# Kernel tuning notes

Measured on AMD Instinct MI355X. Metric: run time of the kernel, lower is better.

Reference implementation:

```python
import jax, jax.numpy as jnp
import numpy as np

B, S, T, D = 4, 2, 1024, 512
H = 8
HD = D // H
EPS = 1e-6
LN_EPS = 1e-5


def setup_inputs() -> dict:
    key = jax.random.key(0)
    ks = jax.random.split(key, 12)
    def lin(k, fan_in, shape):
        bound = 1.0 / np.sqrt(fan_in)
        return jax.random.uniform(k, shape, jnp.float32, -bound, bound)
    return {
        "hidden_states": jax.random.normal(ks[0], (B, S, T, D), jnp.float32),
        "Wq": lin(ks[1], D, (D, D)), "bq": lin(ks[2], D, (D,)),
        "Wk": lin(ks[3], D, (D, D)), "bk": lin(ks[4], D, (D,)),
        "Wv": lin(ks[5], D, (D, D)), "bv": lin(ks[6], D, (D,)),
        "Wo": lin(ks[7], D, (D, D)), "bo": lin(ks[8], D, (D,)),
        "ln_g": jnp.ones((S, D), jnp.float32),
        "ln_b": jnp.zeros((S, D), jnp.float32),
        "gate_alpha": jnp.full((S,), 0.01, jnp.float32),
    }


def _heads(x):
    # [B,T,D] -> [B,H,T,HD]
    return x.reshape(B, T, H, HD).transpose(0, 2, 1, 3)


def _layernorm(x, g, b):
    mu = jnp.mean(x, axis=-1, keepdims=True)
    var = jnp.var(x, axis=-1, keepdims=True)
    return (x - mu) * jax.lax.rsqrt(var + LN_EPS) * g + b


def reference(hidden_states, Wq, bq, Wk, bk, Wv, bv, Wo, bo, ln_g, ln_b, gate_alpha):
    h1, h2 = hidden_states[:, 0], hidden_states[:, 1]  # [B,T,D]
    proj = lambda x, W, b: jnp.einsum('btd,ed->bte', x, W) + b
    Q1, K1, V1 = _heads(proj(h1, Wq, bq)), _heads(proj(h1, Wk, bk)), _heads(proj(h1, Wv, bv))
    Q2, K2, V2 = _heads(proj(h2, Wq, bq)), _heads(proj(h2, Wk, bk)), _heads(proj(h2, Wv, bv))
    scale = 1.0 / np.sqrt(HD)
    L12 = jnp.einsum('bhqd,bhkd->bhqk', Q1, K2) * scale
    L21 = jnp.einsum('bhqd,bhkd->bhqk', Q2, K1) * scale
    S12 = jax.nn.softmax(L12, axis=-1)
    S21 = jax.nn.softmax(L21, axis=-1)
    M = S12 + S21 + EPS
    A12 = S12 / M
    A21 = S21 / M
    H1 = jnp.einsum('bhqk,bhkd->bhqd', A12, V2).transpose(0, 2, 1, 3).reshape(B, T, D)
    H2 = jnp.einsum('bhqk,bhkd->bhqd', A21, V1).transpose(0, 2, 1, 3).reshape(B, T, D)
    H1 = _layernorm(jnp.einsum('btd,ed->bte', H1, Wo) + bo, ln_g[0], ln_b[0])
    H2 = _layernorm(jnp.einsum('btd,ed->bte', H2, Wo) + bo, ln_g[1], ln_b[1])
    attn = jnp.stack([H1, H2], axis=1)  # [B,2,T,D]
    return hidden_states + attn * gate_alpha[None, :, None, None]
```

## Files before the change

### kernel.cpp

```cpp
#include <hip/hip_runtime.h>

#define DEVI __device__ __forceinline__

typedef __bf16 v8bf __attribute__((ext_vector_type(8)));
typedef float  v4f  __attribute__((ext_vector_type(4)));
typedef short  v4s  __attribute__((ext_vector_type(4)));

DEVI unsigned short f2bf(float f) {
  unsigned u = __builtin_bit_cast(unsigned, f);
  u += 0x7fffu + ((u >> 16) & 1u);
  return (unsigned short)(u >> 16);
}
DEVI v4f MFMA32(v8bf a, v8bf b, v4f c) {
  return __builtin_amdgcn_mfma_f32_16x16x32_bf16(a, b, c, 0, 0, 0);
}
DEVI v8bf ldfrag(const unsigned short* p) {
  return __builtin_bit_cast(v8bf, *(const uint4*)p);
}
DEVI v4s ld4s(const unsigned short* p) {
  return __builtin_bit_cast(v4s, *(const uint2*)p);
}
DEVI unsigned pkbf(float lo, float hi) {
  unsigned a = __builtin_bit_cast(unsigned, hi) + 0x8000u;
  unsigned b = __builtin_bit_cast(unsigned, lo) + 0x8000u;
  return __builtin_amdgcn_perm(a, b, 0x07060302u);
}
DEVI float lo2f(unsigned u) { return __builtin_bit_cast(float, u << 16); }
DEVI float hi2f(unsigned u) { return __builtin_bit_cast(float, u & 0xffff0000u); }

#if __has_builtin(__builtin_amdgcn_mfma_f32_16x16x16bf16_1k)
#define HAVE_MFMA16 1
DEVI v4f MFMA16(v4s a, v4s b, v4f c) {
  return __builtin_amdgcn_mfma_f32_16x16x16bf16_1k(a, b, c, 0, 0, 0);
}
#else
#define HAVE_MFMA16 0
#endif

#if __has_builtin(__builtin_amdgcn_global_load_lds)
DEVI void g2l(const unsigned short* g, unsigned short* l) {
  __builtin_amdgcn_global_load_lds(
      (const __attribute__((address_space(1))) unsigned int*)g,
      (__attribute__((address_space(3))) unsigned int*)l, 16, 0, 0);
}
#else
DEVI void g2l(const unsigned short* g, unsigned short* l) {
  *(uint4*)((char*)l + (threadIdx.x & 63) * 16) = *(const uint4*)g;
}
#endif

__global__ __launch_bounds__(256) void convert_kernel(
    const float* __restrict__ X, const float* __restrict__ Wq,
    const float* __restrict__ Wk, const float* __restrict__ Wv,
    const float* __restrict__ Wo, unsigned short* __restrict__ dst)
{
  int t = blockIdx.x * 256 + threadIdx.x;
  int idx = t * 4;
  const float* src;
  if (idx < 4194304) {
    src = X + idx;
  } else {
    int u = idx - 4194304;
    int w = u >> 18;
    const float* W = (w == 0) ? Wq : (w == 1) ? Wk : (w == 2) ? Wv : Wo;
    src = W + (u & 262143);
  }
  float4 f = *(const float4*)src;
  uint2 o;
  o.x = pkbf(f.x, f.y);
  o.y = pkbf(f.z, f.w);
  *(uint2*)&dst[idx] = o;
}

template<int OUTM, int BM>
__global__ __launch_bounds__(256) void gemm_bt(
    const unsigned short* __restrict__ A,
    const unsigned short* __restrict__ W0, const unsigned short* __restrict__ W1,
    const unsigned short* __restrict__ W2,
    const float* __restrict__ b0, const float* __restrict__ b1, const float* __restrict__ b2,
    void* __restrict__ C0, void* __restrict__ C1, void* __restrict__ C2)
{
  const int K = 512, N = 512;
  const int MI = BM / 32;
  const int PER = (BM / 8 + 16) / 4;
  __shared__ unsigned short sAB[(BM + 128) * 64];
  const int z = blockIdx.z;
  const unsigned short* W = (z == 0) ? W0 : (z == 1) ? W1 : W2;
  const float* bias = (z == 0) ? b0 : (z == 1) ? b1 : b2;
  void* C = (z == 0) ? C0 : (z == 1) ? C1 : C2;

  const int tid = threadIdx.x;
  const int lane = tid & 63, wave = tid >> 6;
  const int l15 = lane & 15, quad = lane >> 4, swl = l15 & 7;
  const int lrow = lane >> 3;
  const int lc8 = ((lane & 7) ^ (lrow & 7)) * 8;
  const int wm = (wave >> 1) * (BM / 2), wn = (wave & 1) * 64;
  const int mbase = blockIdx.y * BM, nbase = blockIdx.x * 128;

  const unsigned short* gsrc[PER];
  unsigned short* ldst[PER];
#pragma unroll
  for (int t = 0; t < PER; t++) {
    int c = wave * PER + t;
    ldst[t] = &sAB[c * 512];
    if (c < BM / 8) gsrc[t] = A + (size_t)(mbase + c * 8 + lrow) * K + lc8;
    else            gsrc[t] = W + (size_t)(nbase + (c - BM / 8) * 8 + lrow) * K + lc8;
  }

  v4f acc[MI][4] = {};

  for (int kt = 0; kt < K; kt += 64) {
    __syncthreads();
#pragma unroll
    for (int t = 0; t < PER; t++) g2l(gsrc[t] + kt, ldst[t]);
    __syncthreads();
#pragma unroll
    for (int s = 0; s < 2; s++) {
      v8bf af[MI], bf[4];
#pragma unroll
      for (int i = 0; i < MI; i++)
        af[i] = ldfrag(&sAB[(wm + i * 16 + l15) * 64 + ((s * 4 + quad) ^ swl) * 8]);
#pragma unroll
      for (int j = 0; j < 4; j++)
        bf[j] = ldfrag(&sAB[(BM + wn + j * 16 + l15) * 64 + ((s * 4 + quad) ^ swl) * 8]);
#pragma unroll
      for (int i = 0; i < MI; i++)
#pragma unroll
        for (int j = 0; j < 4; j++)
          acc[i][j] = MFMA32(af[i], bf[j], acc[i][j]);
    }
  }

#pragma unroll
  for (int i = 0; i < MI; i++)
#pragma unroll
    for (int j = 0; j < 4; j++) {
      int row0 = mbase + wm + i * 16 + quad * 4;
      int col = nbase + wn + j * 16 + l15;
      float v[4];
#pragma unroll
      for (int r = 0; r < 4; r++) v[r] = acc[i][j][r] + bias[col];
      if (OUTM == 1) {
#pragma unroll
        for (int r = 0; r < 4; r++) ((float*)C)[(size_t)(row0 + r) * N + col] = v[r];
      } else if (z == 2) {
        int bs = row0 >> 10, t0 = row0 & 1023;
        int hh = col >> 6, hd = col & 63;
        uint2 o;
        o.x = pkbf(v[0], v[1]);
        o.y = pkbf(v[2], v[3]);
        *(uint2*)&((unsigned short*)C)[(size_t)((bs * 8 + hh) * 64 + hd) * 1024 + t0] = o;
      } else {
#pragma unroll
        for (int r = 0; r < 4; r++)
          ((unsigned short*)C)[(size_t)(row0 + r) * N + col] = f2bf(v[r]);
      }
    }
}

__global__ __launch_bounds__(256, 2) void attn_kernel(
    const unsigned short* __restrict__ Qg, const unsigned short* __restrict__ Kg,
    const unsigned short* __restrict__ VTg, unsigned short* __restrict__ Hc)
{
  __shared__ unsigned short sK[2][64][64];
  __shared__ unsigned short sV[2][64][64];

  const int pair = blockIdx.x & 31;
  const int b = pair >> 3, h = pair & 7;
  const int qt = blockIdx.x >> 5;
  const int tid = threadIdx.x;
  const int lane = tid & 63, wave = tid >> 6;
  const int l15 = lane & 15, quad = lane >> 4, swl = l15 & 7;
  const int lrow = lane >> 3;
  const int lc8 = ((lane & 7) ^ (lrow & 7)) * 8;
  const int qbase = qt * 64 + wave * 16;
  const float scale = 0.125f;

  const unsigned short* kgp[2];
  const unsigned short* vgp[2];
#pragma unroll
  for (int st = 0; st < 2; st++) {
    kgp[st] = Kg + (size_t)((b * 2 + st) * 1024) * 512 + h * 64;
    vgp[st] = VTg + (size_t)(((b * 2 + st) * 8 + h) * 64) * 1024;
  }

  v8bf qf[2][2];
#pragma unroll
  for (int d = 0; d < 2; d++)
#pragma unroll
    for (int s = 0; s < 2; s++) {
      int qrow = (b * 2 + d) * 1024 + qbase + l15;
      qf[d][s] = ldfrag(&Qg[(size_t)qrow * 512 + h * 64 + s * 32 + quad * 8]);
    }

  unsigned short* lK = &sK[0][0][0];
  unsigned short* lV = &sV[0][0][0];

  float lacc[2] = {0.f, 0.f};
  {
    const unsigned short* gA[4];
    unsigned short* lA[4];
#pragma unroll
    for (int t = 0; t < 4; t++) {
      int c = wave * 4 + t;
      gA[t] = kgp[c >> 3] + (size_t)((c & 7) * 8 + lrow) * 512 + lc8;
      lA[t] = lK + c * 512;
    }
    for (int kt = 0; kt < 16; kt++) {
      __syncthreads();
#pragma unroll
      for (int t = 0; t < 4; t++) g2l(gA[t] + kt * 32768, lA[t]);
      __syncthreads();
      v4f acc[2][4] = {};
#pragma unroll
      for (int s = 0; s < 2; s++)
#pragma unroll
        for (int d = 0; d < 2; d++)
#pragma unroll
          for (int j = 0; j < 4; j++) {
            v8bf kf = ldfrag(&sK[1 - d][j * 16 + l15][((s * 4 + quad) ^ swl) * 8]);
            acc[d][j] = MFMA32(kf, qf[d][s], acc[d][j]);
          }
#pragma unroll
      for (int d = 0; d < 2; d++)
#pragma unroll
        for (int j = 0; j < 4; j++)
#pragma unroll
          for (int r = 0; r < 4; r++)
            lacc[d] += __expf(acc[d][j][r] * scale);
    }
  }
  float ll[2];
#pragma unroll
  for (int d = 0; d < 2; d++) {
    float v = lacc[d];
    v += __shfl_xor(v, 16);
    v += __shfl_xor(v, 32);
    ll[d] = __logf(v);
  }

  v4f oacc[2][4] = {};
  {
    const unsigned short* gB[8];
    unsigned short* lB[8];
    int stp[8];
#pragma unroll
    for (int t = 0; t < 8; t++) {
      int c = wave * 8 + t;
      if (c < 16) {
        gB[t] = kgp[c >> 3] + (size_t)((c & 7) * 8 + lrow) * 512 + lc8;
        stp[t] = 32768;
        lB[t] = lK + c * 512;
      } else {
        int cv = c - 16;
        gB[t] = vgp[cv >> 3] + (size_t)((cv & 7) * 8 + lrow) * 1024 + lc8;
        stp[t] = 64;
        lB[t] = lV + cv * 512;
      }
    }

    for (int kt = 0; kt < 16; kt++) {
      __syncthreads();
#pragma unroll
      for (int t = 0; t < 8; t++) g2l(gB[t] + kt * stp[t], lB[t]);
      __syncthreads();

      v4f acc[2][4] = {};
#pragma unroll
      for (int s = 0; s < 2; s++)
#pragma unroll
        for (int d = 0; d < 2; d++)
#pragma unroll
          for (int j = 0; j < 4; j++) {
            v8bf kf = ldfrag(&sK[1 - d][j * 16 + l15][((s * 4 + quad) ^ swl) * 8]);
            acc[d][j] = MFMA32(kf, qf[d][s], acc[d][j]);
          }

#pragma unroll
      for (int j = 0; j < 4; j++) {
        float r0[4], r1[4];
#pragma unroll
        for (int r = 0; r < 4; r++) {
          float p0 = __expf(fmaf(acc[0][j][r], scale, -ll[0]));
          float p1 = __expf(fmaf(acc[1][j][r], scale, -ll[1]));
          float ri = __builtin_amdgcn_rcpf(p0 + p1 + 1e-6f);
          r0[r] = p0 * ri;
          r1[r] = p1 * ri;
        }
#if HAVE_MFMA16
        uint2 w0, w1;
        w0.x = pkbf(r0[0], r0[1]); w0.y = pkbf(r0[2], r0[3]);
        w1.x = pkbf(r1[0], r1[1]); w1.y = pkbf(r1[2], r1[3]);
        v4s af0 = __builtin_bit_cast(v4s, w0);
        v4s af1 = __builtin_bit_cast(v4s, w1);
        int vcol = ((j * 2 + (quad >> 1)) ^ swl) * 8 + (quad & 1) * 4;
#pragma unroll
        for (int nt = 0; nt < 4; nt++) {
          v4s vf0 = ld4s(&sV[1][nt * 16 + l15][vcol]);
          v4s vf1 = ld4s(&sV[0][nt * 16 + l15][vcol]);
          oacc[0][nt] = MFMA16(af0, vf0, oacc[0][nt]);
          oacc[1][nt] = MFMA16(af1, vf1, oacc[1][nt]);
        }
#else
#pragma unroll
        for (int d = 0; d < 2; d++) {
          float (&cb)[4] = (d == 0) ? r0 : r1;
          v8bf a;
#pragma unroll
          for (int jj = 0; jj < 8; jj++) {
            int src = l15 + 16 * ((jj >> 2) + (quad & 1) * 2);
            float v = __shfl(cb[jj & 3], src);
            a[jj] = __builtin_bit_cast(__bf16, f2bf(v));
          }
#pragma unroll
          for (int nt = 0; nt < 4; nt++) {
            v8bf vf = ldfrag(&sV[1 - d][nt * 16 + l15]
                               [(((j & 2) * 2 + quad) ^ swl) * 8]);
            oacc[d][nt] = MFMA32(a, vf, oacc[d][nt]);
          }
        }
#endif
      }
    }
  }

#pragma unroll
  for (int d = 0; d < 2; d++)
#pragma unroll
    for (int nt = 0; nt < 4; nt++)
#pragma unroll
      for (int r = 0; r < 4; r++) {
        int row = (b * 2 + d) * 1024 + qbase + quad * 4 + r;
        int col = h * 64 + nt * 16 + l15;
        Hc[(size_t)row * 512 + col] = f2bf(oacc[d][nt][r]);
      }
}

__global__ __launch_bounds__(256) void ln_kernel(
    const unsigned short* __restrict__ Pb, const float* __restrict__ hidden,
    const float* __restrict__ ln_g, const float* __restrict__ ln_b,
    const float* __restrict__ gate, float* __restrict__ out)
{
  const int row = blockIdx.x * 4 + (threadIdx.x >> 6);
  const int s = (row >> 10) & 1;
  const int lane = threadIdx.x & 63;
  const int d0 = lane * 8;

  uint4 up = *(const uint4*)&Pb[(size_t)row * 512 + d0];
  float x[8] = { lo2f(up.x), hi2f(up.x), lo2f(up.y), hi2f(up.y),
                 lo2f(up.z), hi2f(up.z), lo2f(up.w), hi2f(up.w) };
  float s1 = 0.f, s2 = 0.f;
#pragma unroll
  for (int i = 0; i < 8; i++) { s1 += x[i]; s2 += x[i] * x[i]; }
#pragma unroll
  for (int m = 1; m < 64; m <<= 1) { s1 += __shfl_xor(s1, m); s2 += __shfl_xor(s2, m); }
  float mu = s1 * (1.f / 512.f);
  float var = s2 * (1.f / 512.f) - mu * mu;
  float rs = rsqrtf(var + 1e-5f);
  float al = gate[s];

  float4 h0 = *(const float4*)&hidden[(size_t)row * 512 + d0];
  float4 h1 = *(const float4*)&hidden[(size_t)row * 512 + d0 + 4];
  float4 g0 = *(const float4*)&ln_g[s * 512 + d0];
  float4 g1 = *(const float4*)&ln_g[s * 512 + d0 + 4];
  float4 bb0 = *(const float4*)&ln_b[s * 512 + d0];
  float4 bb1 = *(const float4*)&ln_b[s * 512 + d0 + 4];
  float4 o0, o1;
  o0.x = h0.x + ((x[0] - mu) * rs * g0.x + bb0.x) * al;
  o0.y = h0.y + ((x[1] - mu) * rs * g0.y + bb0.y) * al;
  o0.z = h0.z + ((x[2] - mu) * rs * g0.z + bb0.z) * al;
  o0.w = h0.w + ((x[3] - mu) * rs * g0.w + bb0.w) * al;
  o1.x = h1.x + ((x[4] - mu) * rs * g1.x + bb1.x) * al;
  o1.y = h1.y + ((x[5] - mu) * rs * g1.y + bb1.y) * al;
  o1.z = h1.z + ((x[6] - mu) * rs * g1.z + bb1.z) * al;
  o1.w = h1.w + ((x[7] - mu) * rs * g1.w + bb1.w) * al;
  *(float4*)&out[(size_t)row * 512 + d0] = o0;
  *(float4*)&out[(size_t)row * 512 + d0 + 4] = o1;
}

extern "C" void kernel_launch(void* const* d_in, const int* in_sizes, int n_in,
                              void* d_out, int out_size, void* d_ws, size_t ws_size,
                              hipStream_t stream)
{
  const float* hidden = (const float*)d_in[0];
  const float* Wq = (const float*)d_in[1];
  const float* bq = (const float*)d_in[2];
  const float* Wk = (const float*)d_in[3];
  const float* bk = (const float*)d_in[4];
  const float* Wv = (const float*)d_in[5];
  const float* bv = (const float*)d_in[6];
  const float* Wo = (const float*)d_in[7];
  const float* bo = (const float*)d_in[8];
  const float* ln_g = (const float*)d_in[9];
  const float* ln_b = (const float*)d_in[10];
  const float* gate = (const float*)d_in[11];

  unsigned short* U = (unsigned short*)d_ws;
  unsigned short* Xbf = U;
  unsigned short* Wqb = U + 4194304;
  unsigned short* Wkb = U + 4456448;
  unsigned short* Wvb = U + 4718592;
  unsigned short* Wob = U + 4980736;
  unsigned short* Qg  = U + 5242880;
  unsigned short* Kg  = U + 9437184;
  unsigned short* VT  = U + 13631488;
  unsigned short* Hc  = U + 17825792;
  unsigned short* Pb  = (unsigned short*)((char*)d_ws + 44302336);

  convert_kernel<<<dim3(5120), 256, 0, stream>>>(hidden, Wq, Wk, Wv, Wo, Xbf);
  gemm_bt<0, 128><<<dim3(4, 64, 3), 256, 0, stream>>>(Xbf, Wqb, Wkb, Wvb, bq, bk, bv, Qg, Kg, VT);
  attn_kernel<<<dim3(512), 256, 0, stream>>>(Qg, Kg, VT, Hc);
  gemm_bt<0, 64><<<dim3(4, 128, 1), 256, 0, stream>>>(Hc, Wob, Wob, Wob, bo, bo, bo, Pb, Pb, Pb);
  ln_kernel<<<dim3(2048), 256, 0, stream>>>(Pb, hidden, ln_g, ln_b, gate, (float*)d_out);
}
```

Before: 190.3 us.

## Split attention key range across two wave groups and simplify pair normalization

Doubles the attention block to 512 threads. Two groups of four waves each process half of the key sequence for the same 64 queries, and their partial softmax denominators and output accumulators are combined through shared memory. The pair-ratio computation is rewritten algebraically: S12/(S12+S21) becomes a sigmoid of the logit difference, so one exp2 and one reciprocal replace two exps per element. This drops the 1e-6 epsilon term and uses more LDS per block plus an extra reduction pass at the end.

After: 203.6 us. 7.0% more time.

```diff
diff --git a/kernel.cpp b/kernel.cpp
--- a/kernel.cpp
+++ b/kernel.cpp
@@ -27,6 +27,12 @@
 }
 DEVI float lo2f(unsigned u) { return __builtin_bit_cast(float, u << 16); }
 DEVI float hi2f(unsigned u) { return __builtin_bit_cast(float, u & 0xffff0000u); }
+
+#if __has_builtin(__builtin_amdgcn_exp2f)
+DEVI float fexp2(float x) { return __builtin_amdgcn_exp2f(x); }
+#else
+DEVI float fexp2(float x) { return exp2f(x); }
+#endif
 
 #if __has_builtin(__builtin_amdgcn_mfma_f32_16x16x16bf16_1k)
 #define HAVE_MFMA16 1
@@ -158,12 +164,12 @@
     }
 }
 
-__global__ __launch_bounds__(256, 2) void attn_kernel(
+__global__ __launch_bounds__(512, 4) void attn_kernel(
     const unsigned short* __restrict__ Qg, const unsigned short* __restrict__ Kg,
     const unsigned short* __restrict__ VTg, unsigned short* __restrict__ Hc)
 {
-  __shared__ unsigned short sK[2][64][64];
-  __shared__ unsigned short sV[2][64][64];
+  __shared__ unsigned short sT[8][64][64];
+  __shared__ float sL[2][4][2][16];
 
   const int pair = blockIdx.x & 31;
   const int b = pair >> 3, h = pair & 7;
@@ -173,8 +179,9 @@
   const int l15 = lane & 15, quad = lane >> 4, swl = l15 & 7;
   const int lrow = lane >> 3;
   const int lc8 = ((lane & 7) ^ (lrow & 7)) * 8;
-  const int qbase = qt * 64 + wave * 16;
-  const float scale = 0.125f;
+  const int qg = wave & 3, kh = wave >> 2;
+  const int qbase = qt * 64 + qg * 16;
+  const float S2 = 0.125f * 1.44269504f;
 
   const unsigned short* kgp[2];
   const unsigned short* vgp[2];
@@ -193,23 +200,19 @@
       qf[d][s] = ldfrag(&Qg[(size_t)qrow * 512 + h * 64 + s * 32 + quad * 8]);
     }
 
-  unsigned short* lK = &sK[0][0][0];
-  unsigned short* lV = &sV[0][0][0];
-
   float lacc[2] = {0.f, 0.f};
   {
-    const unsigned short* gA[4];
-    unsigned short* lA[4];
-#pragma unroll
-    for (int t = 0; t < 4; t++) {
-      int c = wave * 4 + t;
-      gA[t] = kgp[c >> 3] + (size_t)((c & 7) * 8 + lrow) * 512 + lc8;
-      lA[t] = lK + c * 512;
-    }
-    for (int kt = 0; kt < 16; kt++) {
+    const int tA = (wave >> 1) * 2;
+    const int stA = (wave >> 1) & 1, khA = wave >> 2;
+    const int c0 = (wave & 1) * 4;
+    const unsigned short* gA = kgp[stA] + (size_t)(khA * 512 + c0 * 8 + lrow) * 512 + lc8;
+    unsigned short* lA = &sT[tA][c0 * 8][0];
+
+    for (int kt = 0; kt < 8; kt++) {
       __syncthreads();
 #pragma unroll
-      for (int t = 0; t < 4; t++) g2l(gA[t] + kt * 32768, lA[t]);
+      for (int c = 0; c < 4; c++)
+        g2l(gA + (size_t)(kt * 64 + c * 8) * 512, lA + c * 512);
       __syncthreads();
       v4f acc[2][4] = {};
 #pragma unroll
@@ -218,7 +221,7 @@
         for (int d = 0; d < 2; d++)
 #pragma unroll
           for (int j = 0; j < 4; j++) {
-            v8bf kf = ldfrag(&sK[1 - d][j * 16 + l15][((s * 4 + quad) ^ swl) * 8]);
+            v8bf kf = ldfrag(&sT[kh * 4 + (1 - d) * 2][j * 16 + l15][((s * 4 + quad) ^ swl) * 8]);
             acc[d][j] = MFMA32(kf, qf[d][s], acc[d][j]);
           }
 #pragma unroll
@@ -227,42 +230,45 @@
         for (int j = 0; j < 4; j++)
 #pragma unroll
           for (int r = 0; r < 4; r++)
-            lacc[d] += __expf(acc[d][j][r] * scale);
-    }
-  }
-  float ll[2];
+            lacc[d] += fexp2(acc[d][j][r] * S2);
+    }
+  }
 #pragma unroll
   for (int d = 0; d < 2; d++) {
     float v = lacc[d];
     v += __shfl_xor(v, 16);
     v += __shfl_xor(v, 32);
-    ll[d] = __logf(v);
-  }
+    if (quad == 0) sL[kh][qg][d][l15] = v;
+  }
+  __syncthreads();
+  float ll[2];
+#pragma unroll
+  for (int d = 0; d < 2; d++)
+    ll[d] = __log2f(sL[0][qg][d][l15] + sL[1][qg][d][l15]);
+  const float dll = ll[0] - ll[1];
 
   v4f oacc[2][4] = {};
   {
-    const unsigned short* gB[8];
-    unsigned short* lB[8];
-    int stp[8];
-#pragma unroll
-    for (int t = 0; t < 8; t++) {
-      int c = wave * 8 + t;
-      if (c < 16) {
-        gB[t] = kgp[c >> 3] + (size_t)((c & 7) * 8 + lrow) * 512 + lc8;
-        stp[t] = 32768;
-        lB[t] = lK + c * 512;
-      } else {
-        int cv = c - 16;
-        gB[t] = vgp[cv >> 3] + (size_t)((cv & 7) * 8 + lrow) * 1024 + lc8;
-        stp[t] = 64;
-        lB[t] = lV + cv * 512;
-      }
-    }
-
-    for (int kt = 0; kt < 16; kt++) {
+    const int stw = (wave >> 1) & 1, khw = wave >> 2;
+    const bool isV = wave & 1;
+    const unsigned short* gB;
+    size_t cstep, ktstep;
+    if (isV) {
+      gB = vgp[stw] + (size_t)lrow * 1024 + khw * 512 + lc8;
+      cstep = (size_t)8 * 1024;
+      ktstep = 64;
+    } else {
+      gB = kgp[stw] + (size_t)(khw * 512 + lrow) * 512 + lc8;
+      cstep = (size_t)8 * 512;
+      ktstep = (size_t)64 * 512;
+    }
+    unsigned short* lB = &sT[wave][0][0];
+
+    for (int kt = 0; kt < 8; kt++) {
       __syncthreads();
 #pragma unroll
-      for (int t = 0; t < 8; t++) g2l(gB[t] + kt * stp[t], lB[t]);
+      for (int c = 0; c < 8; c++)
+        g2l(gB + (size_t)kt * ktstep + c * cstep, lB + c * 512);
       __syncthreads();
 
       v4f acc[2][4] = {};
@@ -272,7 +278,7 @@
         for (int d = 0; d < 2; d++)
 #pragma unroll
           for (int j = 0; j < 4; j++) {
-            v8bf kf = ldfrag(&sK[1 - d][j * 16 + l15][((s * 4 + quad) ^ swl) * 8]);
+            v8bf kf = ldfrag(&sT[kh * 4 + (1 - d) * 2][j * 16 + l15][((s * 4 + quad) ^ swl) * 8]);
             acc[d][j] = MFMA32(kf, qf[d][s], acc[d][j]);
           }
 
@@ -281,11 +287,10 @@
         float r0[4], r1[4];
 #pragma unroll
         for (int r = 0; r < 4; r++) {
-          float p0 = __expf(fmaf(acc[0][j][r], scale, -ll[0]));
-          float p1 = __expf(fmaf(acc[1][j][r], scale, -ll[1]));
-          float ri = __builtin_amdgcn_rcpf(p0 + p1 + 1e-6f);
-          r0[r] = p0 * ri;
-          r1[r] = p1 * ri;
+          float t = fmaf(acc[1][j][r] - acc[0][j][r], S2, dll);
+          float ri = __builtin_amdgcn_rcpf(1.f + fexp2(t));
+          r0[r] = ri;
+          r1[r] = 1.f - ri;
         }
 #if HAVE_MFMA16
         uint2 w0, w1;
@@ -296,8 +301,8 @@
         int vcol = ((j * 2 + (quad >> 1)) ^ swl) * 8 + (quad & 1) * 4;
 #pragma unroll
         for (int nt = 0; nt < 4; nt++) {
-          v4s vf0 = ld4s(&sV[1][nt * 16 + l15][vcol]);
-          v4s vf1 = ld4s(&sV[0][nt * 16 + l15][vcol]);
+          v4s vf0 = ld4s(&sT[kh * 4 + 3][nt * 16 + l15][vcol]);
+          v4s vf1 = ld4s(&sT[kh * 4 + 1][nt * 16 + l15][vcol]);
           oacc[0][nt] = MFMA16(af0, vf0, oacc[0][nt]);
           oacc[1][nt] = MFMA16(af1, vf1, oacc[1][nt]);
         }
@@ -314,7 +319,7 @@
           }
 #pragma unroll
           for (int nt = 0; nt < 4; nt++) {
-            v8bf vf = ldfrag(&sV[1 - d][nt * 16 + l15]
+            v8bf vf = ldfrag(&sT[kh * 4 + (1 - d) * 2 + 1][nt * 16 + l15]
                                [(((j & 2) * 2 + quad) ^ swl) * 8]);
             oacc[d][nt] = MFMA32(a, vf, oacc[d][nt]);
           }
@@ -324,16 +329,31 @@
     }
   }
 
-#pragma unroll
-  for (int d = 0; d < 2; d++)
-#pragma unroll
-    for (int nt = 0; nt < 4; nt++)
-#pragma unroll
-      for (int r = 0; r < 4; r++) {
-        int row = (b * 2 + d) * 1024 + qbase + quad * 4 + r;
-        int col = h * 64 + nt * 16 + l15;
-        Hc[(size_t)row * 512 + col] = f2bf(oacc[d][nt][r]);
-      }
+  __syncthreads();
+  float* sO = (float*)&sT[0][0][0];
+  if (kh == 1) {
+#pragma unroll
+    for (int d = 0; d < 2; d++)
+#pragma unroll
+      for (int nt = 0; nt < 4; nt++)
+#pragma unroll
+        for (int r = 0; r < 4; r++)
+          sO[(size_t)((d * 4 + nt) * 4 + r) * 256 + qg * 64 + lane] = oacc[d][nt][r];
+  }
+  __syncthreads();
+  if (kh == 0) {
+#pragma unroll
+    for (int d = 0; d < 2; d++)
+#pragma unroll
+      for (int nt = 0; nt < 4; nt++)
+#pragma unroll
+        for (int r = 0; r < 4; r++) {
+          float v = oacc[d][nt][r] + sO[(size_t)((d * 4 + nt) * 4 + r) * 256 + qg * 64 + lane];
+          int row = (b * 2 + d) * 1024 + qbase + quad * 4 + r;
+          int col = h * 64 + nt * 16 + l15;
+          Hc[(size_t)row * 512 + col] = f2bf(v);
+        }
+  }
 }
 
 __global__ __launch_bounds__(256) void ln_kernel(
@@ -409,7 +429,7 @@
 
   convert_kernel<<<dim3(5120), 256, 0, stream>>>(hidden, Wq, Wk, Wv, Wo, Xbf);
   gemm_bt<0, 128><<<dim3(4, 64, 3), 256, 0, stream>>>(Xbf, Wqb, Wkb, Wvb, bq, bk, bv, Qg, Kg, VT);
-  attn_kernel<<<dim3(512), 256, 0, stream>>>(Qg, Kg, VT, Hc);
+  attn_kernel<<<dim3(512), 512, 0, stream>>>(Qg, Kg, VT, Hc);
   gemm_bt<0, 64><<<dim3(4, 128, 1), 256, 0, stream>>>(Hc, Wob, Wob, Wob, bo, bo, bo, Pb, Pb, Pb);
   ln_kernel<<<dim3(2048), 256, 0, stream>>>(Pb, hidden, ln_g, ln_b, gate, (float*)d_out);
 }
```

## Double-buffer K/V LDS tiles with prefetch and simplify pair-normalized softmax via exp2

Applied to the files above, without the earlier changes.

The K and V shared-memory tiles become double-buffered in both attention passes. The next tile's global-to-LDS loads are issued before the current tile is computed, which leaves one barrier per iteration instead of two. Separately, the pair ratio S12/(S12+S21) is rewritten as a sigmoid of the logit difference in base 2, so each element needs one exp2 and one reciprocal instead of two exps. This drops the epsilon term, and doubling the LDS footprint may limit occupancy.

New measurement: 180.7 us. 5.0% less time.

```diff
diff --git a/kernel.cpp b/kernel.cpp
--- a/kernel.cpp
+++ b/kernel.cpp
@@ -27,6 +27,12 @@
 }
 DEVI float lo2f(unsigned u) { return __builtin_bit_cast(float, u << 16); }
 DEVI float hi2f(unsigned u) { return __builtin_bit_cast(float, u & 0xffff0000u); }
+
+#if __has_builtin(__builtin_amdgcn_exp2f)
+DEVI float fexp2(float x) { return __builtin_amdgcn_exp2f(x); }
+#else
+DEVI float fexp2(float x) { return exp2f(x); }
+#endif
 
 #if __has_builtin(__builtin_amdgcn_mfma_f32_16x16x16bf16_1k)
 #define HAVE_MFMA16 1
@@ -162,8 +168,8 @@
     const unsigned short* __restrict__ Qg, const unsigned short* __restrict__ Kg,
     const unsigned short* __restrict__ VTg, unsigned short* __restrict__ Hc)
 {
-  __shared__ unsigned short sK[2][64][64];
-  __shared__ unsigned short sV[2][64][64];
+  __shared__ unsigned short sK[2][2][64][64];
+  __shared__ unsigned short sV[2][2][64][64];
 
   const int pair = blockIdx.x & 31;
   const int b = pair >> 3, h = pair & 7;
@@ -174,7 +180,7 @@
   const int lrow = lane >> 3;
   const int lc8 = ((lane & 7) ^ (lrow & 7)) * 8;
   const int qbase = qt * 64 + wave * 16;
-  const float scale = 0.125f;
+  const float S2 = 0.125f * 1.44269504f;
 
   const unsigned short* kgp[2];
   const unsigned short* vgp[2];
@@ -193,24 +199,28 @@
       qf[d][s] = ldfrag(&Qg[(size_t)qrow * 512 + h * 64 + s * 32 + quad * 8]);
     }
 
-  unsigned short* lK = &sK[0][0][0];
-  unsigned short* lV = &sV[0][0][0];
-
   float lacc[2] = {0.f, 0.f};
   {
     const unsigned short* gA[4];
-    unsigned short* lA[4];
+    unsigned short* lA[2][4];
 #pragma unroll
     for (int t = 0; t < 4; t++) {
       int c = wave * 4 + t;
       gA[t] = kgp[c >> 3] + (size_t)((c & 7) * 8 + lrow) * 512 + lc8;
-      lA[t] = lK + c * 512;
-    }
+      lA[0][t] = &sK[0][c >> 3][(c & 7) * 8][0];
+      lA[1][t] = &sK[1][c >> 3][(c & 7) * 8][0];
+    }
+#pragma unroll
+    for (int t = 0; t < 4; t++) g2l(gA[t], lA[0][t]);
+
     for (int kt = 0; kt < 16; kt++) {
       __syncthreads();
-#pragma unroll
-      for (int t = 0; t < 4; t++) g2l(gA[t] + kt * 32768, lA[t]);
-      __syncthreads();
+      if (kt < 15) {
+#pragma unroll
+        for (int t = 0; t < 4; t++)
+          g2l(gA[t] + (size_t)(kt + 1) * 32768, lA[(kt + 1) & 1][t]);
+      }
+      const int bu = kt & 1;
       v4f acc[2][4] = {};
 #pragma unroll
       for (int s = 0; s < 2; s++)
@@ -218,7 +228,7 @@
         for (int d = 0; d < 2; d++)
 #pragma unroll
           for (int j = 0; j < 4; j++) {
-            v8bf kf = ldfrag(&sK[1 - d][j * 16 + l15][((s * 4 + quad) ^ swl) * 8]);
+            v8bf kf = ldfrag(&sK[bu][1 - d][j * 16 + l15][((s * 4 + quad) ^ swl) * 8]);
             acc[d][j] = MFMA32(kf, qf[d][s], acc[d][j]);
           }
 #pragma unroll
@@ -227,7 +237,7 @@
         for (int j = 0; j < 4; j++)
 #pragma unroll
           for (int r = 0; r < 4; r++)
-            lacc[d] += __expf(acc[d][j][r] * scale);
+            lacc[d] += fexp2(acc[d][j][r] * S2);
     }
   }
   float ll[2];
@@ -236,34 +246,43 @@
     float v = lacc[d];
     v += __shfl_xor(v, 16);
     v += __shfl_xor(v, 32);
-    ll[d] = __logf(v);
-  }
+    ll[d] = __log2f(v);
+  }
+  const float dll = ll[0] - ll[1];
 
   v4f oacc[2][4] = {};
   {
     const unsigned short* gB[8];
-    unsigned short* lB[8];
-    int stp[8];
+    unsigned short* lB[2][8];
+    size_t stp[8];
 #pragma unroll
     for (int t = 0; t < 8; t++) {
       int c = wave * 8 + t;
       if (c < 16) {
         gB[t] = kgp[c >> 3] + (size_t)((c & 7) * 8 + lrow) * 512 + lc8;
         stp[t] = 32768;
-        lB[t] = lK + c * 512;
+        lB[0][t] = &sK[0][c >> 3][(c & 7) * 8][0];
+        lB[1][t] = &sK[1][c >> 3][(c & 7) * 8][0];
       } else {
         int cv = c - 16;
         gB[t] = vgp[cv >> 3] + (size_t)((cv & 7) * 8 + lrow) * 1024 + lc8;
         stp[t] = 64;
-        lB[t] = lV + cv * 512;
-      }
-    }
+        lB[0][t] = &sV[0][cv >> 3][(cv & 7) * 8][0];
+        lB[1][t] = &sV[1][cv >> 3][(cv & 7) * 8][0];
+      }
+    }
+    __syncthreads();
+#pragma unroll
+    for (int t = 0; t < 8; t++) g2l(gB[t], lB[0][t]);
 
     for (int kt = 0; kt < 16; kt++) {
       __syncthreads();
-#pragma unroll
-      for (int t = 0; t < 8; t++) g2l(gB[t] + kt * stp[t], lB[t]);
-      __syncthreads();
+      if (kt < 15) {
+#pragma unroll
+        for (int t = 0; t < 8; t++)
+          g2l(gB[t] + (size_t)(kt + 1) * stp[t], lB[(kt + 1) & 1][t]);
+      }
+      const int bu = kt & 1;
 
       v4f acc[2][4] = {};
 #pragma unroll
@@ -272,7 +291,7 @@
         for (int d = 0; d < 2; d++)
 #pragma unroll
           for (int j = 0; j < 4; j++) {
-            v8bf kf = ldfrag(&sK[1 - d][j * 16 + l15][((s * 4 + quad) ^ swl) * 8]);
+            v8bf kf = ldfrag(&sK[bu][1 - d][j * 16 + l15][((s * 4 + quad) ^ swl) * 8]);
             acc[d][j] = MFMA32(kf, qf[d][s], acc[d][j]);
           }
 
@@ -281,11 +300,10 @@
         float r0[4], r1[4];
 #pragma unroll
         for (int r = 0; r < 4; r++) {
-          float p0 = __expf(fmaf(acc[0][j][r], scale, -ll[0]));
-          float p1 = __expf(fmaf(acc[1][j][r], scale, -ll[1]));
-          float ri = __builtin_amdgcn_rcpf(p0 + p1 + 1e-6f);
-          r0[r] = p0 * ri;
-          r1[r] = p1 * ri;
+          float t = fmaf(acc[1][j][r] - acc[0][j][r], S2, dll);
+          float ri = __builtin_amdgcn_rcpf(1.f + fexp2(t));
+          r0[r] = ri;
+          r1[r] = 1.f - ri;
         }
 #if HAVE_MFMA16
         uint2 w0, w1;
@@ -296,8 +314,8 @@
         int vcol = ((j * 2 + (quad >> 1)) ^ swl) * 8 + (quad & 1) * 4;
 #pragma unroll
         for (int nt = 0; nt < 4; nt++) {
-          v4s vf0 = ld4s(&sV[1][nt * 16 + l15][vcol]);
-          v4s vf1 = ld4s(&sV[0][nt * 16 + l15][vcol]);
+          v4s vf0 = ld4s(&sV[bu][1][nt * 16 + l15][vcol]);
+          v4s vf1 = ld4s(&sV[bu][0][nt * 16 + l15][vcol]);
           oacc[0][nt] = MFMA16(af0, vf0, oacc[0][nt]);
           oacc[1][nt] = MFMA16(af1, vf1, oacc[1][nt]);
         }
@@ -314,7 +332,7 @@
           }
 #pragma unroll
           for (int nt = 0; nt < 4; nt++) {
-            v8bf vf = ldfrag(&sV[1 - d][nt * 16 + l15]
+            v8bf vf = ldfrag(&sV[bu][1 - d][nt * 16 + l15]
                                [(((j & 2) * 2 + quad) ^ swl) * 8]);
             oacc[d][nt] = MFMA32(a, vf, oacc[d][nt]);
           }
```
